# Kernel tuning notes

Measured on AMD Instinct MI355X. Metric: run time of the kernel, lower is better.

The kernel has to match this reference:

```python
import jax, jax.numpy as jnp
import numpy as np

# Per-layer (in_dim, hidden) for the 6 stacked LSTM layers:
# rnn_inp: (1,64),(64,64),(64,64); rnn_out: (64,1),(1,1),(1,1)
_LAYER_DIMS = [(1, 64), (64, 64), (64, 64), (64, 1), (1, 1), (1, 1)]
_LAYER_NAMES = ['a0', 'a1', 'a2', 'b0', 'b1', 'b2']


def _lstm_layer(x, w_ih, w_hh, b_ih, b_hh):
    """Single unidirectional LSTM layer, PyTorch gate order (i, f, g, o).
    x: [B, T, Din]; w_ih: [4H, Din]; w_hh: [4H, H]; biases: [4H]. Returns [B, T, H]."""
    H = w_hh.shape[1]
    B = x.shape[0]
    # Input projection for all timesteps at once (one big GEMM).
    pre = jnp.einsum('btd,gd->btg', x, w_ih) + b_ih + b_hh  # [B, T, 4H]
    pre_t = jnp.swapaxes(pre, 0, 1)  # [T, B, 4H]

    def step(carry, xt):
        h, c = carry
        gates = xt + h @ w_hh.T  # [B, 4H]
        i, f, g, o = jnp.split(gates, 4, axis=-1)
        i = jax.nn.sigmoid(i)
        f = jax.nn.sigmoid(f)
        g = jnp.tanh(g)
        o = jax.nn.sigmoid(o)
        c = f * c + i * g
        h = o * jnp.tanh(c)
        return (h, c), h

    h0 = jnp.zeros((B, H), x.dtype)
    (_, _), hs = jax.lax.scan(step, (h0, h0), pre_t)  # hs: [T, B, H]
    return jnp.swapaxes(hs, 0, 1)


def setup_inputs() -> dict:
    key = jax.random.key(0)
    B, T = 256, 512
    inp = {}
    k, key = jax.random.split(key)
    inp['x'] = jax.random.normal(k, (B, T, 1), dtype=jnp.float32)
    for name, (din, h) in zip(_LAYER_NAMES, _LAYER_DIMS):
        s = 1.0 / np.sqrt(h)  # PyTorch LSTM init scale U(-1/sqrt(H), 1/sqrt(H))
        k1, k2, k3, k4, key = jax.random.split(key, 5)
        inp[f'w_ih_{name}'] = jax.random.uniform(k1, (4 * h, din), jnp.float32, -s, s)
        inp[f'w_hh_{name}'] = jax.random.uniform(k2, (4 * h, h), jnp.float32, -s, s)
        inp[f'b_ih_{name}'] = jax.random.uniform(k3, (4 * h,), jnp.float32, -s, s)
        inp[f'b_hh_{name}'] = jax.random.uniform(k4, (4 * h,), jnp.float32, -s, s)
    return inp


def reference(x,
              w_ih_a0, w_hh_a0, b_ih_a0, b_hh_a0,
              w_ih_a1, w_hh_a1, b_ih_a1, b_hh_a1,
              w_ih_a2, w_hh_a2, b_ih_a2, b_hh_a2,
              w_ih_b0, w_hh_b0, b_ih_b0, b_hh_b0,
              w_ih_b1, w_hh_b1, b_ih_b1, b_hh_b1,
              w_ih_b2, w_hh_b2, b_ih_b2, b_hh_b2):
    layers = [
        (w_ih_a0, w_hh_a0, b_ih_a0, b_hh_a0),
        (w_ih_a1, w_hh_a1, b_ih_a1, b_hh_a1),
        (w_ih_a2, w_hh_a2, b_ih_a2, b_hh_a2),
        (w_ih_b0, w_hh_b0, b_ih_b0, b_hh_b0),
        (w_ih_b1, w_hh_b1, b_ih_b1, b_hh_b1),
        (w_ih_b2, w_hh_b2, b_ih_b2, b_hh_b2),
    ]
    h = x
    for w_ih, w_hh, b_ih, b_hh in layers:
        h = _lstm_layer(h, w_ih, w_hh, b_ih, b_hh)
    # activation between the two LSTM stacks is identity (activation_type='identity')
    return h  # [B, T, 1]
```

## Files before the change

### kernel.cpp

```cpp
#include <hip/hip_runtime.h>


#define BB 256
#define TT 512
#define CH 4
#define NS 8

typedef _Float16 v2h __attribute__((ext_vector_type(2)));

__device__ __forceinline__ float sig_(float x) {
  return __builtin_amdgcn_rcpf(1.f + __builtin_amdgcn_exp2f(-1.44269504f * x));
}
__device__ __forceinline__ float tanh_(float x) {
  return __builtin_fmaf(2.f, __builtin_amdgcn_rcpf(1.f + __builtin_amdgcn_exp2f(-2.88539008f * x)), -1.f);
}

template <int K>
__device__ __forceinline__ float qb_(float v) {
  return __int_as_float(__builtin_amdgcn_update_dpp(
      0, __float_as_int(v), (K | (K << 2) | (K << 4) | (K << 6)), 0xF, 0xF, true));
}

__device__ __forceinline__ void ldsbar_() {
  asm volatile("s_waitcnt lgkmcnt(0)\n\ts_barrier" ::: "memory");
}

#if __has_builtin(__builtin_amdgcn_fdot2)
#define FDOT2(acc, a, b) (acc) = __builtin_amdgcn_fdot2((a), (b), (acc), false)
#else
#define FDOT2(acc, a, b) \
  (acc) = __builtin_fmaf((float)(a)[0], (float)(b)[0], \
          __builtin_fmaf((float)(a)[1], (float)(b)[1], (acc)))
#endif
#define KEEPP(a) asm volatile("" : "+v"(a))
#define PIN32(w)                                                            \
  do {                                                                      \
    _Pragma("unroll") for (int _i = 0; _i < 32; ++_i) KEEPP((w)[_i]);       \
  } while (0)

__device__ __forceinline__ v2h bc2h_(int v) { return __builtin_bit_cast(v2h, v); }

__device__ __forceinline__ void load_h64(const _Float16* p, v2h hv[32]) {
  const int4* hp = reinterpret_cast<const int4*>(p);
#pragma unroll
  for (int i = 0; i < 8; ++i) {
    int4 blk = hp[i];
    hv[4 * i + 0] = bc2h_(blk.x);
    hv[4 * i + 1] = bc2h_(blk.y);
    hv[4 * i + 2] = bc2h_(blk.z);
    hv[4 * i + 3] = bc2h_(blk.w);
  }
}

__device__ __forceinline__ void load_row16(const float* src, v2h dst[32]) {
  const float4* p = reinterpret_cast<const float4*>(src);
#pragma unroll
  for (int i = 0; i < 16; ++i) {
    float4 v = p[i];
    dst[2 * i]     = v2h{(_Float16)v.x, (_Float16)v.y};
    dst[2 * i + 1] = v2h{(_Float16)v.z, (_Float16)v.w};
  }
}

__device__ __forceinline__ void dot4_(const v2h w[4][32], const v2h hv[32],
                                      float& p0, float& p1, float& p2, float& p3) {
  float a0 = p0, a1 = p1, a2 = p2, a3 = p3;
  float b0 = 0.f, b1 = 0.f, b2 = 0.f, b3 = 0.f;
#pragma unroll
  for (int j = 0; j < 32; j += 2) {
    FDOT2(a0, w[0][j], hv[j]);         FDOT2(a1, w[1][j], hv[j]);
    FDOT2(a2, w[2][j], hv[j]);         FDOT2(a3, w[3][j], hv[j]);
    FDOT2(b0, w[0][j + 1], hv[j + 1]); FDOT2(b1, w[1][j + 1], hv[j + 1]);
    FDOT2(b2, w[2][j + 1], hv[j + 1]); FDOT2(b3, w[3][j + 1], hv[j + 1]);
  }
  p0 = a0 + b0; p1 = a1 + b1; p2 = a2 + b2; p3 = a3 + b3;
}

__device__ __forceinline__ void dot2g_(const v2h* w0, const v2h* w1,
                                       const v2h hv[32], float& p0, float& p1) {
  float a0 = 0.f, a1 = 0.f, b0 = 0.f, b1 = 0.f;
#pragma unroll
  for (int j = 0; j < 32; j += 2) {
    FDOT2(a0, w0[j], hv[j]);         FDOT2(a1, w1[j], hv[j]);
    FDOT2(b0, w0[j + 1], hv[j + 1]); FDOT2(b1, w1[j + 1], hv[j + 1]);
  }
  p0 = a0 + b0; p1 = a1 + b1;
}

__global__ __attribute__((amdgpu_flat_work_group_size(512, 512),
                          amdgpu_waves_per_eu(1, 2)))
void lstm_pipe_k(
    const float* __restrict__ x,
    const float* __restrict__ wih_a0, const float* __restrict__ whh_a0,
    const float* __restrict__ bih_a0, const float* __restrict__ bhh_a0,
    const float* __restrict__ wih_a1, const float* __restrict__ whh_a1,
    const float* __restrict__ bih_a1, const float* __restrict__ bhh_a1,
    const float* __restrict__ wih_a2, const float* __restrict__ whh_a2,
    const float* __restrict__ bih_a2, const float* __restrict__ bhh_a2,
    const float* __restrict__ wih_b0, const float* __restrict__ whh_b0,
    const float* __restrict__ bih_b0, const float* __restrict__ bhh_b0,
    const float* __restrict__ wih_b1, const float* __restrict__ whh_b1,
    const float* __restrict__ bih_b1, const float* __restrict__ bhh_b1,
    const float* __restrict__ wih_b2, const float* __restrict__ whh_b2,
    const float* __restrict__ bih_b2, const float* __restrict__ bhh_b2,
    float* __restrict__ out)
{
  asm volatile("" ::: "v190", "v191");

  const int b = blockIdx.x;
  const int tid = threadIdx.x;
  const int wave = tid >> 6;
  const int lane = tid & 63;

  __shared__ __align__(16) _Float16 hh[3][NS][64];
  __shared__ __align__(16) float pj[2][NS][256];
  __shared__ float xs[TT];

  for (int i = tid; i < TT; i += 512) xs[i] = x[(size_t)b * TT + i];
  for (int i = tid; i < 3 * NS * 64 / 2; i += 512) reinterpret_cast<int*>(hh)[i] = 0;

  v2h wt[4][32];
  float bias[4] = {0.f, 0.f, 0.f, 0.f};
  float wi0_[4] = {0.f, 0.f, 0.f, 0.f};
  float whb0[4] = {}, wi1b[4] = {}, wh1b[4] = {}, bb1[4] = {},
        wi2b[4] = {}, wh2b[4] = {}, bb2[4] = {};

  if (wave == 0) {
#pragma unroll
    for (int q = 0; q < 4; ++q) {
      const int row = q * 64 + lane;
      load_row16(whh_a0 + row * 64, wt[q]);
      bias[q] = bih_a0[row] + bhh_a0[row];
      wi0_[q] = wih_a0[row];
    }
    PIN32(wt[0]); PIN32(wt[1]); PIN32(wt[2]); PIN32(wt[3]);
  } else if (wave == 1) {
#pragma unroll
    for (int q = 0; q < 4; ++q) {
      const int row = q * 64 + lane;
      load_row16(whh_a1 + row * 64, wt[q]);
      bias[q] = bih_a1[row] + bhh_a1[row];
    }
    PIN32(wt[0]); PIN32(wt[1]); PIN32(wt[2]); PIN32(wt[3]);
  } else if (wave == 2) {
#pragma unroll
    for (int q = 0; q < 4; ++q) {
      const int row = q * 64 + lane;
      load_row16(whh_a2 + row * 64, wt[q]);
      bias[q] = bih_a2[row] + bhh_a2[row];
    }
    PIN32(wt[0]); PIN32(wt[1]); PIN32(wt[2]); PIN32(wt[3]);
  } else if (wave == 3) {
    const int q = lane & 3;
    load_row16(wih_b0 + q * 64, wt[0]);
    bias[0] = bih_b0[q] + bhh_b0[q];
#pragma unroll
    for (int k = 0; k < 4; ++k) {
      whb0[k] = whh_b0[k];
      wi1b[k] = wih_b1[k]; wh1b[k] = whh_b1[k]; bb1[k] = bih_b1[k] + bhh_b1[k];
      wi2b[k] = wih_b2[k]; wh2b[k] = whh_b2[k]; bb2[k] = bih_b2[k] + bhh_b2[k];
    }
    PIN32(wt[0]);
  } else if (wave == 4) {
#pragma unroll
    for (int q = 0; q < 2; ++q) load_row16(wih_a1 + (q * 64 + lane) * 64, wt[q]);
    PIN32(wt[0]); PIN32(wt[1]);
  } else if (wave == 5) {
#pragma unroll
    for (int q = 0; q < 2; ++q) load_row16(wih_a1 + ((q + 2) * 64 + lane) * 64, wt[q]);
    PIN32(wt[0]); PIN32(wt[1]);
  } else if (wave == 6) {
#pragma unroll
    for (int q = 0; q < 2; ++q) load_row16(wih_a2 + (q * 64 + lane) * 64, wt[q]);
    PIN32(wt[0]); PIN32(wt[1]);
  } else {
#pragma unroll
    for (int q = 0; q < 2; ++q) load_row16(wih_a2 + ((q + 2) * 64 + lane) * 64, wt[q]);
    PIN32(wt[0]); PIN32(wt[1]);
  }
  __syncthreads();

  float c = 0.f;
  float h0b = 0.f, c0b = 0.f, h1b = 0.f, c1b = 0.f, h2b = 0.f, c2b = 0.f;

  const int NE = TT / CH + 5;
  for (int e = 0; e < NE; ++e) {
    if (wave == 0) {
      const int t0 = e * CH;
      if (t0 < TT) {
        __builtin_amdgcn_s_setprio(1);
        for (int s = 0; s < CH; ++s) {
          const int t = t0 + s;
          v2h hv[32];
          load_h64(&hh[0][(t + NS - 1) & (NS - 1)][0], hv);
          const float xv = xs[t];
          float p0 = bias[0], p1 = bias[1], p2 = bias[2], p3 = bias[3];
          dot4_(wt, hv, p0, p1, p2, p3);
          p0 = __builtin_fmaf(wi0_[0], xv, p0);
          p1 = __builtin_fmaf(wi0_[1], xv, p1);
          p2 = __builtin_fmaf(wi0_[2], xv, p2);
          p3 = __builtin_fmaf(wi0_[3], xv, p3);
          float gi = sig_(p0), gf = sig_(p1), gg = tanh_(p2), go = sig_(p3);
          c = __builtin_fmaf(gf, c, gi * gg);
          hh[0][t & (NS - 1)][lane] = (_Float16)(go * tanh_(c));
          asm volatile("s_waitcnt lgkmcnt(0)" ::: "memory");
        }
        __builtin_amdgcn_s_setprio(0);
      }
    } else if (wave == 1) {
      const int t0 = (e - 2) * CH;
      if (t0 >= 0 && t0 < TT) {
        __builtin_amdgcn_s_setprio(1);
        for (int s = 0; s < CH; ++s) {
          const int t = t0 + s;
          v2h hv[32];
          load_h64(&hh[1][(t + NS - 1) & (NS - 1)][0], hv);
          float4 pr = *reinterpret_cast<const float4*>(&pj[0][t & (NS - 1)][lane * 4]);
          float p0 = bias[0], p1 = bias[1], p2 = bias[2], p3 = bias[3];
          dot4_(wt, hv, p0, p1, p2, p3);
          p0 += pr.x; p1 += pr.y; p2 += pr.z; p3 += pr.w;
          float gi = sig_(p0), gf = sig_(p1), gg = tanh_(p2), go = sig_(p3);
          c = __builtin_fmaf(gf, c, gi * gg);
          hh[1][t & (NS - 1)][lane] = (_Float16)(go * tanh_(c));
          asm volatile("s_waitcnt lgkmcnt(0)" ::: "memory");
        }
        __builtin_amdgcn_s_setprio(0);
      }
    } else if (wave == 2) {
      const int t0 = (e - 4) * CH;
      if (t0 >= 0 && t0 < TT) {
        __builtin_amdgcn_s_setprio(1);
        for (int s = 0; s < CH; ++s) {
          const int t = t0 + s;
          v2h hv[32];
          load_h64(&hh[2][(t + NS - 1) & (NS - 1)][0], hv);
          float4 pr = *reinterpret_cast<const float4*>(&pj[1][t & (NS - 1)][lane * 4]);
          float p0 = bias[0], p1 = bias[1], p2 = bias[2], p3 = bias[3];
          dot4_(wt, hv, p0, p1, p2, p3);
          p0 += pr.x; p1 += pr.y; p2 += pr.z; p3 += pr.w;
          float gi = sig_(p0), gf = sig_(p1), gg = tanh_(p2), go = sig_(p3);
          c = __builtin_fmaf(gf, c, gi * gg);
          hh[2][t & (NS - 1)][lane] = (_Float16)(go * tanh_(c));
          asm volatile("s_waitcnt lgkmcnt(0)" ::: "memory");
        }
        __builtin_amdgcn_s_setprio(0);
      }
    } else if (wave == 3) {
      const int t0 = (e - 5) * CH;
      if (t0 >= 0 && t0 < TT) {
        for (int s = 0; s < CH; ++s) {
          const int t = t0 + s;
          v2h hv[32];
          load_h64(&hh[2][t & (NS - 1)][0], hv);
          float pga = bias[0], pgb = 0.f;
#pragma unroll
          for (int j = 0; j < 32; j += 2) {
            FDOT2(pga, wt[0][j], hv[j]);
            FDOT2(pgb, wt[0][j + 1], hv[j + 1]);
          }
          float pg = pga + pgb;
          float p_i = qb_<0>(pg), p_f = qb_<1>(pg), p_g = qb_<2>(pg), p_o = qb_<3>(pg);
          float i0 = sig_(__builtin_fmaf(whb0[0], h0b, p_i));
          float f0 = sig_(__builtin_fmaf(whb0[1], h0b, p_f));
          float g0 = tanh_(__builtin_fmaf(whb0[2], h0b, p_g));
          float o0 = sig_(__builtin_fmaf(whb0[3], h0b, p_o));
          c0b = __builtin_fmaf(f0, c0b, i0 * g0);
          h0b = o0 * tanh_(c0b);
          float i1 = sig_(bb1[0] + __builtin_fmaf(wi1b[0], h0b, wh1b[0] * h1b));
          float f1 = sig_(bb1[1] + __builtin_fmaf(wi1b[1], h0b, wh1b[1] * h1b));
          float g1 = tanh_(bb1[2] + __builtin_fmaf(wi1b[2], h0b, wh1b[2] * h1b));
          float o1 = sig_(bb1[3] + __builtin_fmaf(wi1b[3], h0b, wh1b[3] * h1b));
          c1b = __builtin_fmaf(f1, c1b, i1 * g1);
          h1b = o1 * tanh_(c1b);
          float i2 = sig_(bb2[0] + __builtin_fmaf(wi2b[0], h1b, wh2b[0] * h2b));
          float f2 = sig_(bb2[1] + __builtin_fmaf(wi2b[1], h1b, wh2b[1] * h2b));
          float g2 = tanh_(bb2[2] + __builtin_fmaf(wi2b[2], h1b, wh2b[2] * h2b));
          float o2 = sig_(bb2[3] + __builtin_fmaf(wi2b[3], h1b, wh2b[3] * h2b));
          c2b = __builtin_fmaf(f2, c2b, i2 * g2);
          h2b = o2 * tanh_(c2b);
          if (lane == 0) out[(size_t)b * TT + t] = h2b;
        }
      }
    } else if (wave == 4) {
      const int t0 = (e - 1) * CH;
      if (t0 >= 0 && t0 < TT) {
        for (int s = 0; s < CH; ++s) {
          const int t = t0 + s;
          v2h hv[32];
          load_h64(&hh[0][t & (NS - 1)][0], hv);
          float p0, p1;
          dot2g_(wt[0], wt[1], hv, p0, p1);
          *reinterpret_cast<float2*>(&pj[0][t & (NS - 1)][lane * 4]) = float2{p0, p1};
        }
      }
    } else if (wave == 5) {
      const int t0 = (e - 1) * CH;
      if (t0 >= 0 && t0 < TT) {
        for (int s = 0; s < CH; ++s) {
          const int t = t0 + s;
          v2h hv[32];
          load_h64(&hh[0][t & (NS - 1)][0], hv);
          float p2, p3;
          dot2g_(wt[0], wt[1], hv, p2, p3);
          *reinterpret_cast<float2*>(&pj[0][t & (NS - 1)][lane * 4 + 2]) = float2{p2, p3};
        }
      }
    } else if (wave == 6) {
      const int t0 = (e - 3) * CH;
      if (t0 >= 0 && t0 < TT) {
        for (int s = 0; s < CH; ++s) {
          const int t = t0 + s;
          v2h hv[32];
          load_h64(&hh[1][t & (NS - 1)][0], hv);
          float p0, p1;
          dot2g_(wt[0], wt[1], hv, p0, p1);
          *reinterpret_cast<float2*>(&pj[1][t & (NS - 1)][lane * 4]) = float2{p0, p1};
        }
      }
    } else {
      const int t0 = (e - 3) * CH;
      if (t0 >= 0 && t0 < TT) {
        for (int s = 0; s < CH; ++s) {
          const int t = t0 + s;
          v2h hv[32];
          load_h64(&hh[1][t & (NS - 1)][0], hv);
          float p2, p3;
          dot2g_(wt[0], wt[1], hv, p2, p3);
          *reinterpret_cast<float2*>(&pj[1][t & (NS - 1)][lane * 4 + 2]) = float2{p2, p3};
        }
      }
    }
    ldsbar_();
  }
}

extern "C" void kernel_launch(void* const* d_in, const int* in_sizes, int n_in,
                              void* d_out, int out_size, void* d_ws, size_t ws_size,
                              hipStream_t stream) {
  const float* x      = (const float*)d_in[0];
  const float* wih_a0 = (const float*)d_in[1];
  const float* whh_a0 = (const float*)d_in[2];
  const float* bih_a0 = (const float*)d_in[3];
  const float* bhh_a0 = (const float*)d_in[4];
  const float* wih_a1 = (const float*)d_in[5];
  const float* whh_a1 = (const float*)d_in[6];
  const float* bih_a1 = (const float*)d_in[7];
  const float* bhh_a1 = (const float*)d_in[8];
  const float* wih_a2 = (const float*)d_in[9];
  const float* whh_a2 = (const float*)d_in[10];
  const float* bih_a2 = (const float*)d_in[11];
  const float* bhh_a2 = (const float*)d_in[12];
  const float* wih_b0 = (const float*)d_in[13];
  const float* whh_b0 = (const float*)d_in[14];
  const float* bih_b0 = (const float*)d_in[15];
  const float* bhh_b0 = (const float*)d_in[16];
  const float* wih_b1 = (const float*)d_in[17];
  const float* whh_b1 = (const float*)d_in[18];
  const float* bih_b1 = (const float*)d_in[19];
  const float* bhh_b1 = (const float*)d_in[20];
  const float* wih_b2 = (const float*)d_in[21];
  const float* whh_b2 = (const float*)d_in[22];
  const float* bih_b2 = (const float*)d_in[23];
  const float* bhh_b2 = (const float*)d_in[24];
  float* out = (float*)d_out;

  lstm_pipe_k<<<BB, 512, 0, stream>>>(
      x,
      wih_a0, whh_a0, bih_a0, bhh_a0,
      wih_a1, whh_a1, bih_a1, bhh_a1,
      wih_a2, whh_a2, bih_a2, bhh_a2,
      wih_b0, whh_b0, bih_b0, bhh_b0,
      wih_b1, whh_b1, bih_b1, bhh_b1,
      wih_b2, whh_b2, bih_b2, bhh_b2,
      out);
}
```

Before: 401.5 us.

## Use packed fp16 FMA accumulation, larger time chunks, and prefetched projections

Replaces the fdot2 fp32-accumulating dot products with packed half-precision FMAs (v_pk_fma_f16) accumulating in fp16, reduced to fp32 with a final dot against ones. It also doubles the chunk size and ring depth so there are fewer block barriers, prefetches the next input projection one step ahead, and drops the per-step lgkmcnt waits after LDS stores. Each barrier is meant to cover more work and the serial dependency chain per step gets shorter. Accumulating 64-term dot products in fp16 loses precision and may push the output past tolerance. Removing the waits relies on the same wave reading its own LDS writes in order.

```diff
diff --git a/kernel.cpp b/kernel.cpp
--- a/kernel.cpp
+++ b/kernel.cpp
@@ -3,8 +3,8 @@
 
 #define BB 256
 #define TT 512
-#define CH 4
-#define NS 8
+#define CH 8
+#define NS 16
 
 typedef _Float16 v2h __attribute__((ext_vector_type(2)));
 
@@ -32,6 +32,13 @@
   (acc) = __builtin_fmaf((float)(a)[0], (float)(b)[0], \
           __builtin_fmaf((float)(a)[1], (float)(b)[1], (acc)))
 #endif
+
+#if __has_builtin(__builtin_elementwise_fma)
+#define PKFMA(acc, a, b) (acc) = __builtin_elementwise_fma((a), (b), (acc))
+#else
+#define PKFMA(acc, a, b) (acc) += (a) * (b)
+#endif
+
 #define KEEPP(a) asm volatile("" : "+v"(a))
 #define PIN32(w)                                                            \
   do {                                                                      \
@@ -62,33 +69,38 @@
   }
 }
 
-__device__ __forceinline__ void dot4_(const v2h w[4][32], const v2h hv[32],
-                                      float& p0, float& p1, float& p2, float& p3) {
-  float a0 = p0, a1 = p1, a2 = p2, a3 = p3;
-  float b0 = 0.f, b1 = 0.f, b2 = 0.f, b3 = 0.f;
+__device__ __forceinline__ void dot4pk_(const v2h w[4][32], const v2h hv[32],
+                                        float& p0, float& p1, float& p2, float& p3) {
+  v2h a0{}, a1{}, a2{}, a3{}, b0{}, b1{}, b2{}, b3{};
 #pragma unroll
   for (int j = 0; j < 32; j += 2) {
-    FDOT2(a0, w[0][j], hv[j]);         FDOT2(a1, w[1][j], hv[j]);
-    FDOT2(a2, w[2][j], hv[j]);         FDOT2(a3, w[3][j], hv[j]);
-    FDOT2(b0, w[0][j + 1], hv[j + 1]); FDOT2(b1, w[1][j + 1], hv[j + 1]);
-    FDOT2(b2, w[2][j + 1], hv[j + 1]); FDOT2(b3, w[3][j + 1], hv[j + 1]);
-  }
-  p0 = a0 + b0; p1 = a1 + b1; p2 = a2 + b2; p3 = a3 + b3;
-}
-
-__device__ __forceinline__ void dot2g_(const v2h* w0, const v2h* w1,
-                                       const v2h hv[32], float& p0, float& p1) {
-  float a0 = 0.f, a1 = 0.f, b0 = 0.f, b1 = 0.f;
+    PKFMA(a0, w[0][j], hv[j]);         PKFMA(a1, w[1][j], hv[j]);
+    PKFMA(a2, w[2][j], hv[j]);         PKFMA(a3, w[3][j], hv[j]);
+    PKFMA(b0, w[0][j + 1], hv[j + 1]); PKFMA(b1, w[1][j + 1], hv[j + 1]);
+    PKFMA(b2, w[2][j + 1], hv[j + 1]); PKFMA(b3, w[3][j + 1], hv[j + 1]);
+  }
+  const v2h one = {(_Float16)1.f, (_Float16)1.f};
+  FDOT2(p0, a0, one); FDOT2(p1, a1, one); FDOT2(p2, a2, one); FDOT2(p3, a3, one);
+  FDOT2(p0, b0, one); FDOT2(p1, b1, one); FDOT2(p2, b2, one); FDOT2(p3, b3, one);
+}
+
+__device__ __forceinline__ void dot2gpk_(const v2h* w0, const v2h* w1,
+                                         const v2h hv[32], float& p0, float& p1) {
+  v2h a0{}, a1{}, b0{}, b1{};
 #pragma unroll
   for (int j = 0; j < 32; j += 2) {
-    FDOT2(a0, w0[j], hv[j]);         FDOT2(a1, w1[j], hv[j]);
-    FDOT2(b0, w0[j + 1], hv[j + 1]); FDOT2(b1, w1[j + 1], hv[j + 1]);
-  }
-  p0 = a0 + b0; p1 = a1 + b1;
+    PKFMA(a0, w0[j], hv[j]);         PKFMA(a1, w1[j], hv[j]);
+    PKFMA(b0, w0[j + 1], hv[j + 1]); PKFMA(b1, w1[j + 1], hv[j + 1]);
+  }
+  const v2h one = {(_Float16)1.f, (_Float16)1.f};
+  float r0 = 0.f, r1 = 0.f;
+  FDOT2(r0, a0, one); FDOT2(r1, a1, one);
+  FDOT2(r0, b0, one); FDOT2(r1, b1, one);
+  p0 = r0; p1 = r1;
 }
 
 __global__ __attribute__((amdgpu_flat_work_group_size(512, 512),
-                          amdgpu_waves_per_eu(1, 2)))
+                          amdgpu_waves_per_eu(2, 2)))
 void lstm_pipe_k(
     const float* __restrict__ x,
     const float* __restrict__ wih_a0, const float* __restrict__ whh_a0,
@@ -105,7 +117,7 @@
     const float* __restrict__ bih_b2, const float* __restrict__ bhh_b2,
     float* __restrict__ out)
 {
-  asm volatile("" ::: "v190", "v191");
+  asm volatile("" ::: "v204", "v205", "v206", "v207");
 
   const int b = blockIdx.x;
   const int tid = threadIdx.x;
@@ -195,7 +207,7 @@
           load_h64(&hh[0][(t + NS - 1) & (NS - 1)][0], hv);
           const float xv = xs[t];
           float p0 = bias[0], p1 = bias[1], p2 = bias[2], p3 = bias[3];
-          dot4_(wt, hv, p0, p1, p2, p3);
+          dot4pk_(wt, hv, p0, p1, p2, p3);
           p0 = __builtin_fmaf(wi0_[0], xv, p0);
           p1 = __builtin_fmaf(wi0_[1], xv, p1);
           p2 = __builtin_fmaf(wi0_[2], xv, p2);
@@ -203,7 +215,6 @@
           float gi = sig_(p0), gf = sig_(p1), gg = tanh_(p2), go = sig_(p3);
           c = __builtin_fmaf(gf, c, gi * gg);
           hh[0][t & (NS - 1)][lane] = (_Float16)(go * tanh_(c));
-          asm volatile("s_waitcnt lgkmcnt(0)" ::: "memory");
         }
         __builtin_amdgcn_s_setprio(0);
       }
@@ -211,18 +222,21 @@
       const int t0 = (e - 2) * CH;
       if (t0 >= 0 && t0 < TT) {
         __builtin_amdgcn_s_setprio(1);
+        float4 pr = *reinterpret_cast<const float4*>(&pj[0][t0 & (NS - 1)][lane * 4]);
         for (int s = 0; s < CH; ++s) {
           const int t = t0 + s;
           v2h hv[32];
           load_h64(&hh[1][(t + NS - 1) & (NS - 1)][0], hv);
-          float4 pr = *reinterpret_cast<const float4*>(&pj[0][t & (NS - 1)][lane * 4]);
+          float4 prn = pr;
+          if (s + 1 < CH)
+            prn = *reinterpret_cast<const float4*>(&pj[0][(t + 1) & (NS - 1)][lane * 4]);
           float p0 = bias[0], p1 = bias[1], p2 = bias[2], p3 = bias[3];
-          dot4_(wt, hv, p0, p1, p2, p3);
+          dot4pk_(wt, hv, p0, p1, p2, p3);
           p0 += pr.x; p1 += pr.y; p2 += pr.z; p3 += pr.w;
           float gi = sig_(p0), gf = sig_(p1), gg = tanh_(p2), go = sig_(p3);
           c = __builtin_fmaf(gf, c, gi * gg);
           hh[1][t & (NS - 1)][lane] = (_Float16)(go * tanh_(c));
-          asm volatile("s_waitcnt lgkmcnt(0)" ::: "memory");
+          pr = prn;
         }
         __builtin_amdgcn_s_setprio(0);
       }
@@ -230,18 +244,21 @@
       const int t0 = (e - 4) * CH;
       if (t0 >= 0 && t0 < TT) {
         __builtin_amdgcn_s_setprio(1);
+        float4 pr = *reinterpret_cast<const float4*>(&pj[1][t0 & (NS - 1)][lane * 4]);
         for (int s = 0; s < CH; ++s) {
           const int t = t0 + s;
           v2h hv[32];
           load_h64(&hh[2][(t + NS - 1) & (NS - 1)][0], hv);
-          float4 pr = *reinterpret_cast<const float4*>(&pj[1][t & (NS - 1)][lane * 4]);
+          float4 prn = pr;
+          if (s + 1 < CH)
+            prn = *reinterpret_cast<const float4*>(&pj[1][(t + 1) & (NS - 1)][lane * 4]);
           float p0 = bias[0], p1 = bias[1], p2 = bias[2], p3 = bias[3];
-          dot4_(wt, hv, p0, p1, p2, p3);
+          dot4pk_(wt, hv, p0, p1, p2, p3);
           p0 += pr.x; p1 += pr.y; p2 += pr.z; p3 += pr.w;
           float gi = sig_(p0), gf = sig_(p1), gg = tanh_(p2), go = sig_(p3);
           c = __builtin_fmaf(gf, c, gi * gg);
           hh[2][t & (NS - 1)][lane] = (_Float16)(go * tanh_(c));
-          asm volatile("s_waitcnt lgkmcnt(0)" ::: "memory");
+          pr = prn;
         }
         __builtin_amdgcn_s_setprio(0);
       }
@@ -252,13 +269,16 @@
           const int t = t0 + s;
           v2h hv[32];
           load_h64(&hh[2][t & (NS - 1)][0], hv);
-          float pga = bias[0], pgb = 0.f;
+          v2h pa{}, pb{};
 #pragma unroll
           for (int j = 0; j < 32; j += 2) {
-            FDOT2(pga, wt[0][j], hv[j]);
-            FDOT2(pgb, wt[0][j + 1], hv[j + 1]);
+            PKFMA(pa, wt[0][j], hv[j]);
+            PKFMA(pb, wt[0][j + 1], hv[j + 1]);
           }
-          float pg = pga + pgb;
+          const v2h one = {(_Float16)1.f, (_Float16)1.f};
+          float pg = bias[0];
+          FDOT2(pg, pa, one);
+          FDOT2(pg, pb, one);
           float p_i = qb_<0>(pg), p_f = qb_<1>(pg), p_g = qb_<2>(pg), p_o = qb_<3>(pg);
           float i0 = sig_(__builtin_fmaf(whb0[0], h0b, p_i));
           float f0 = sig_(__builtin_fmaf(whb0[1], h0b, p_f));
@@ -289,7 +309,7 @@
           v2h hv[32];
           load_h64(&hh[0][t & (NS - 1)][0], hv);
           float p0, p1;
-          dot2g_(wt[0], wt[1], hv, p0, p1);
+          dot2gpk_(wt[0], wt[1], hv, p0, p1);
           *reinterpret_cast<float2*>(&pj[0][t & (NS - 1)][lane * 4]) = float2{p0, p1};
         }
       }
@@ -301,7 +321,7 @@
           v2h hv[32];
           load_h64(&hh[0][t & (NS - 1)][0], hv);
           float p2, p3;
-          dot2g_(wt[0], wt[1], hv, p2, p3);
+          dot2gpk_(wt[0], wt[1], hv, p2, p3);
           *reinterpret_cast<float2*>(&pj[0][t & (NS - 1)][lane * 4 + 2]) = float2{p2, p3};
         }
       }
@@ -313,7 +333,7 @@
           v2h hv[32];
           load_h64(&hh[1][t & (NS - 1)][0], hv);
           float p0, p1;
-          dot2g_(wt[0], wt[1], hv, p0, p1);
+          dot2gpk_(wt[0], wt[1], hv, p0, p1);
           *reinterpret_cast<float2*>(&pj[1][t & (NS - 1)][lane * 4]) = float2{p0, p1};
         }
       }
@@ -325,7 +345,7 @@
           v2h hv[32];
           load_h64(&hh[1][t & (NS - 1)][0], hv);
           float p2, p3;
-          dot2g_(wt[0], wt[1], hv, p2, p3);
+          dot2gpk_(wt[0], wt[1], hv, p2, p3);
           *reinterpret_cast<float2*>(&pj[1][t & (NS - 1)][lane * 4 + 2]) = float2{p2, p3};
         }
       }
```

After: 401.1 us. No clear change (-0.1%).
